# Performance work log

Hardware: AMD Instinct MI355X
Metric: run time of the kernel (lower is better)

The kernel has to match this reference:

```python
import jax, jax.numpy as jnp
import numpy as np
from jax.scipy.linalg import expm

HIDDEN = 1024
STATE = 64
INTER = 4096
EPS = 1e-06
DT_MIN, DT_MAX = 0.001, 0.1


def rmsnorm(x, w, eps=EPS):
    var = jnp.mean(x * x, axis=-1, keepdims=True)
    return x * jax.lax.rsqrt(var + eps) * w


def setup_inputs() -> dict:
    key = jax.random.key(0)
    ks = jax.random.split(key, 10)
    hidden_states = jax.random.normal(ks[0], (4, 2048, HIDDEN), dtype=jnp.float32)
    A = jax.random.normal(ks[1], (STATE, STATE), dtype=jnp.float32) * 0.01
    B = jax.random.normal(ks[2], (STATE, HIDDEN), dtype=jnp.float32) * 0.01
    C = jax.random.normal(ks[3], (HIDDEN, STATE), dtype=jnp.float32) * 0.01
    D = jnp.ones((HIDDEN,), dtype=jnp.float32)
    log_dt = jax.random.uniform(ks[4], (HIDDEN,), dtype=jnp.float32) * (np.log(DT_MAX) - np.log(DT_MIN)) + np.log(DT_MIN)
    s = 1.0 / np.sqrt(HIDDEN)
    w_gate = jax.random.uniform(ks[5], (INTER, HIDDEN), minval=-s, maxval=s, dtype=jnp.float32)
    w_up = jax.random.uniform(ks[6], (INTER, HIDDEN), minval=-s, maxval=s, dtype=jnp.float32)
    s2 = 1.0 / np.sqrt(INTER)
    w_down = jax.random.uniform(ks[7], (HIDDEN, INTER), minval=-s2, maxval=s2, dtype=jnp.float32)
    ln1_w = jnp.ones((HIDDEN,), dtype=jnp.float32)
    ln2_w = jnp.ones((HIDDEN,), dtype=jnp.float32)
    return {"hidden_states": hidden_states, "A": A, "B": B, "C": C, "D": D,
            "log_dt": log_dt, "w_gate": w_gate, "w_up": w_up, "w_down": w_down,
            "ln1_w": ln1_w, "ln2_w": ln2_w}


def ssm(x, A, B, C, D, log_dt):
    # x: (batch, seq, hidden)
    dt = jnp.exp(log_dt)                    # (hidden,)
    A_bar = expm(A * jnp.mean(dt))          # (state, state)
    B_bar = B * dt[None, :]                 # (state, hidden)

    def step(state, x_t):
        # state: (batch, state); x_t: (batch, hidden)
        state = state @ A_bar.T + x_t @ B_bar.T
        out = state @ C.T + D * x_t
        return state, out

    x_t = jnp.swapaxes(x, 0, 1)             # (seq, batch, hidden)
    init = jnp.zeros((x.shape[0], A.shape[0]), dtype=x.dtype)
    _, ys = jax.lax.scan(step, init, x_t)
    return jnp.swapaxes(ys, 0, 1)           # (batch, seq, hidden)


def reference(hidden_states, A, B, C, D, log_dt, w_gate, w_up, w_down, ln1_w, ln2_w):
    # pre-norm SSM mixer + residual
    residual = hidden_states
    h = rmsnorm(hidden_states, ln1_w)
    h = ssm(h, A, B, C, D, log_dt)
    h = residual + h
    # pre-norm SwiGLU FFN + residual
    residual = h
    hn = rmsnorm(h, ln2_w)
    gate = hn @ w_gate.T
    up = hn @ w_up.T
    ffn = (jax.nn.silu(gate) * up) @ w_down.T
    return residual + ffn
```

## Files before the change

kernel.cpp:

```cpp
#include <hip/hip_runtime.h>
#include <hip/hip_bf16.h>
#include <math.h>

typedef __attribute__((ext_vector_type(8))) short short8;
typedef __attribute__((ext_vector_type(4))) float f32x4;
typedef __attribute__((ext_vector_type(4))) int int4v;
typedef __attribute__((ext_vector_type(8))) int int8v;

__device__ __forceinline__ unsigned short f2b(float x) {
  union { float f; unsigned int u; } v; v.f = x;
  unsigned int r = v.u + 0x7fffu + ((v.u >> 16) & 1u);
  return (unsigned short)(r >> 16);
}
__device__ __forceinline__ float b2f(unsigned short u) {
  union { unsigned int u; float f; } v; v.u = ((unsigned int)u) << 16;
  return v.f;
}
__device__ __forceinline__ unsigned char f2f8_sw(float x) {
  float a = fabsf(x);
  unsigned char s = (x < 0.f) ? 0x80 : 0x00;
  if (a >= 464.f) return s | 0x7E;
  union { float f; unsigned u; } v; v.f = a;
  int e = (int)(v.u >> 23) - 127;
  if (e < -6) {
    int q = (int)rintf(a * 512.f);
    if (q >= 8) return s | 0x08;
    return s | (unsigned char)q;
  }
  unsigned mant = v.u & 0x7FFFFF;
  unsigned keep = mant >> 20;
  unsigned rest = mant & 0xFFFFF;
  if (rest > 0x80000u || (rest == 0x80000u && (keep & 1))) keep++;
  unsigned exp8 = (unsigned)(e + 7);
  if (keep == 8) { keep = 0; exp8++; }
  if (exp8 >= 15 && keep >= 7) return s | 0x7E;
  return s | (unsigned char)((exp8 << 3) | keep);
}
#if __has_builtin(__builtin_amdgcn_cvt_pk_fp8_f32)
__device__ __forceinline__ unsigned char f2f8(float x) {
  return (unsigned char)(__builtin_amdgcn_cvt_pk_fp8_f32(x, x, 0, false) & 0xFF);
}
__device__ __forceinline__ unsigned int f8pack4(float a, float b, float c, float d) {
  int w0 = __builtin_amdgcn_cvt_pk_fp8_f32(a, b, 0, false);
  return (unsigned int)__builtin_amdgcn_cvt_pk_fp8_f32(c, d, w0, true);
}
#else
__device__ __forceinline__ unsigned char f2f8(float x) { return f2f8_sw(x); }
__device__ __forceinline__ unsigned int f8pack4(float a, float b, float c, float d) {
  return (unsigned)f2f8_sw(a) | ((unsigned)f2f8_sw(b) << 8) |
         ((unsigned)f2f8_sw(c) << 16) | ((unsigned)f2f8_sw(d) << 24);
}
#endif
__device__ __forceinline__ void async_ld16(const void* g, void* l) {
  __builtin_amdgcn_global_load_lds(
      (const __attribute__((address_space(1))) void*)g,
      (__attribute__((address_space(3))) void*)l, 16, 0, 0);
}

__device__ __forceinline__ f32x4 mx8(int8v a, int8v b, f32x4 c) {
#if __has_builtin(__builtin_amdgcn_mfma_scale_f32_16x16x128_f8f6f4)
  return __builtin_amdgcn_mfma_scale_f32_16x16x128_f8f6f4(
      a, b, c, 0, 0, 0, 0x7F7F7F7F, 0, 0x7F7F7F7F);
#else
  union { int8v v; long l[4]; } av, bv; av.v = a; bv.v = b;
#pragma unroll
  for (int j = 0; j < 4; j++)
    c = __builtin_amdgcn_mfma_f32_16x16x32_fp8_fp8(av.l[j], bv.l[j], c, 0, 0, 0);
  return c;
#endif
}

__device__ __forceinline__ int8v rd8(const unsigned char* tb, int r, int q) {
  union { int8v v; int4v h[2]; } x;
  x.h[0] = *(const int4v*)(tb + (size_t)((r << 3) + ((2 * q)     ^ (r & 7))) * 16);
  x.h[1] = *(const int4v*)(tb + (size_t)((r << 3) + ((2 * q + 1) ^ (r & 7))) * 16);
  return x.v;
}

__global__ __launch_bounds__(1024) void prep_combo(
    const float* __restrict__ A, const float* __restrict__ logdt,
    float* __restrict__ Abar, float* __restrict__ A64,
    const float* __restrict__ B, const float* __restrict__ Cm,
    unsigned short* __restrict__ Bb, unsigned short* __restrict__ Cb) {
  __shared__ float red[16];
  __shared__ float Ms[4096], T[4096], P[4096];
  if (blockIdx.x != 0) {
    const size_t NB = 65536, NC = 65536;
    size_t base = (size_t)(blockIdx.x - 1) * 1024 + threadIdx.x;
    size_t stride = (size_t)(gridDim.x - 1) * 1024;
    for (size_t id = base; id < NB + NC; id += stride) {
      if (id < NB) { int k = (int)(id & 1023); Bb[id] = f2b(B[id] * expf(logdt[k])); }
      else Cb[id - NB] = f2b(Cm[id - NB]);
    }
    return;
  }
  const int tid = threadIdx.x;
  const int c = tid & 63;
  const int w = tid >> 6;
  float e = expf(logdt[tid]);
#pragma unroll
  for (int off = 32; off > 0; off >>= 1) e += __shfl_down(e, off);
  if (c == 0) red[w] = e;
  __syncthreads();
  if (tid == 0) {
    float s = 0.f;
    for (int i = 0; i < 16; i++) s += red[i];
    red[0] = s * (1.f / 1024.f);
  }
  __syncthreads();
  const float mdt = red[0];
  {
    float m0 = A[tid] * mdt, m1 = A[tid + 1024] * mdt,
          m2 = A[tid + 2048] * mdt, m3 = A[tid + 3072] * mdt;
    Ms[tid] = m0; Ms[tid + 1024] = m1; Ms[tid + 2048] = m2; Ms[tid + 3072] = m3;
    T[tid] = m0; T[tid + 1024] = m1; T[tid + 2048] = m2; T[tid + 3072] = m3;
    P[tid] = m0 + ((tid >> 6) == (tid & 63) ? 1.f : 0.f);
    P[tid + 1024] = m1 + (((tid + 1024) >> 6) == ((tid + 1024) & 63) ? 1.f : 0.f);
    P[tid + 2048] = m2 + (((tid + 2048) >> 6) == ((tid + 2048) & 63) ? 1.f : 0.f);
    P[tid + 3072] = m3 + (((tid + 3072) >> 6) == ((tid + 3072) & 63) ? 1.f : 0.f);
  }
  __syncthreads();
  float colM[64];
#pragma unroll
  for (int j = 0; j < 64; j++) colM[j] = Ms[j * 64 + c];
  for (int k = 2; k <= 6; k++) {
    const float inv = 1.f / (float)k;
    float accs[4];
#pragma unroll
    for (int i = 0; i < 4; i++) {
      const int r = w + 16 * i;
      const float4* Trow = (const float4*)(T + r * 64);
      float a0 = 0.f, a1 = 0.f, a2 = 0.f, a3 = 0.f;
#pragma unroll
      for (int j4 = 0; j4 < 16; j4++) {
        const float4 t = Trow[j4];
        a0 += t.x * colM[4 * j4 + 0]; a1 += t.y * colM[4 * j4 + 1];
        a2 += t.z * colM[4 * j4 + 2]; a3 += t.w * colM[4 * j4 + 3];
      }
      accs[i] = ((a0 + a1) + (a2 + a3)) * inv;
    }
    __syncthreads();
#pragma unroll
    for (int i = 0; i < 4; i++) {
      const int r = w + 16 * i;
      T[r * 64 + c] = accs[i];
      P[r * 64 + c] += accs[i];
    }
    __syncthreads();
  }
#pragma unroll
  for (int i = 0; i < 4; i++) {
    const int r = w + 16 * i;
    Abar[r * 64 + c] = P[r * 64 + c];
    T[r * 64 + c] = P[r * 64 + c];
  }
  __syncthreads();
  for (int sq = 0; sq < 6; sq++) {
    float colT[64];
#pragma unroll
    for (int j = 0; j < 64; j++) colT[j] = T[j * 64 + c];
    float accs[4];
#pragma unroll
    for (int i = 0; i < 4; i++) {
      const int r = w + 16 * i;
      const float4* Trow = (const float4*)(T + r * 64);
      float a0 = 0.f, a1 = 0.f, a2 = 0.f, a3 = 0.f;
#pragma unroll
      for (int j4 = 0; j4 < 16; j4++) {
        const float4 t = Trow[j4];
        a0 += t.x * colT[4 * j4 + 0]; a1 += t.y * colT[4 * j4 + 1];
        a2 += t.z * colT[4 * j4 + 2]; a3 += t.w * colT[4 * j4 + 3];
      }
      accs[i] = (a0 + a1) + (a2 + a3);
    }
    __syncthreads();
#pragma unroll
    for (int i = 0; i < 4; i++) T[(w + 16 * i) * 64 + c] = accs[i];
    __syncthreads();
  }
#pragma unroll
  for (int i = 0; i < 4; i++) {
    const int r = w + 16 * i;
    A64[r * 64 + c] = T[r * 64 + c];
  }
}

__global__ __launch_bounds__(256) void rmsnorm_bf16(
    const float* __restrict__ x, const float* __restrict__ w,
    unsigned short* __restrict__ out) {
  const size_t row = blockIdx.x;
  const int tid = threadIdx.x;
  const float4 v = ((const float4*)(x + row * 1024))[tid];
  float ss = v.x * v.x + v.y * v.y + v.z * v.z + v.w * v.w;
#pragma unroll
  for (int off = 32; off > 0; off >>= 1) ss += __shfl_down(ss, off);
  __shared__ float wsum[4];
  if ((tid & 63) == 0) wsum[tid >> 6] = ss;
  __syncthreads();
  const float tot = wsum[0] + wsum[1] + wsum[2] + wsum[3];
  const float rs = rsqrtf(tot * (1.f / 1024.f) + 1e-6f);
  const float4 wv = ((const float4*)w)[tid];
  ushort4 o;
  o.x = f2b(v.x * rs * wv.x); o.y = f2b(v.y * rs * wv.y);
  o.z = f2b(v.z * rs * wv.z); o.w = f2b(v.w * rs * wv.w);
  ((ushort4*)(out + row * 1024))[tid] = o;
}

__global__ __launch_bounds__(256) void rmsnorm_f8(
    const float* __restrict__ x, const float* __restrict__ w,
    unsigned int* __restrict__ out) {
  const size_t row = blockIdx.x;
  const int tid = threadIdx.x;
  const float4 v = ((const float4*)(x + row * 1024))[tid];
  float ss = v.x * v.x + v.y * v.y + v.z * v.z + v.w * v.w;
#pragma unroll
  for (int off = 32; off > 0; off >>= 1) ss += __shfl_down(ss, off);
  __shared__ float wsum[4];
  if ((tid & 63) == 0) wsum[tid >> 6] = ss;
  __syncthreads();
  const float tot = wsum[0] + wsum[1] + wsum[2] + wsum[3];
  const float rs = rsqrtf(tot * (1.f / 1024.f) + 1e-6f);
  const float4 wv = ((const float4*)w)[tid];
  out[row * 256 + tid] =
      f8pack4(v.x * rs * wv.x, v.y * rs * wv.y, v.z * rs * wv.z, v.w * rs * wv.w);
}

template <int STORE_S>
__global__ __launch_bounds__(256) void scan_combo(
    const float* __restrict__ U, const float* __restrict__ Abar,
    const float* __restrict__ carry, float* __restrict__ zend,
    unsigned short* __restrict__ S,
    const float* __restrict__ csrc, unsigned char* __restrict__ cdst, size_t ccount) {
  constexpr int SCAN_BLOCKS = 32;
  __shared__ float s[4][64];
  if (blockIdx.x >= SCAN_BLOCKS) {
    size_t base = (size_t)(blockIdx.x - SCAN_BLOCKS) * 256 + threadIdx.x;
    size_t stride = (size_t)(gridDim.x - SCAN_BLOCKS) * 256;
    for (size_t id = base; id < ccount; id += stride)
      cdst[id] = f2f8(csrc[id] * 64.f);
    return;
  }
  const int wave = threadIdx.x >> 6, i = threadIdx.x & 63;
  const int task = blockIdx.x * 4 + wave;
  const int b = task >> 5, c = task & 31;
  float a[64];
#pragma unroll
  for (int j = 0; j < 64; j++) a[j] = Abar[i * 64 + j];
  float cur = STORE_S ? carry[(b * 32 + c) * 64 + i] : 0.f;
  const float* Ub = U + ((size_t)(b * 2048 + c * 64)) * 64;
  for (int t = 0; t < 64; t++) {
    s[wave][i] = cur;
    __syncthreads();
    const float u = Ub[t * 64 + i];
    const float4* s4 = (const float4*)s[wave];
    float a0 = u, a1 = 0.f, a2 = 0.f, a3 = 0.f;
#pragma unroll
    for (int j = 0; j < 16; j++) {
      float4 v = s4[j];
      a0 += a[4 * j + 0] * v.x; a1 += a[4 * j + 1] * v.y;
      a2 += a[4 * j + 2] * v.z; a3 += a[4 * j + 3] * v.w;
    }
    cur = (a0 + a1) + (a2 + a3);
    __syncthreads();
    if (STORE_S) S[((size_t)(b * 2048 + c * 64 + t)) * 64 + i] = f2b(cur);
  }
  if (!STORE_S) zend[(b * 32 + c) * 64 + i] = cur;
}

__global__ __launch_bounds__(256) void carry_combo(
    const float* __restrict__ zend, const float* __restrict__ A64,
    float* __restrict__ carry,
    const float* __restrict__ csrc, unsigned char* __restrict__ cdst, size_t ccount) {
  __shared__ float s[4][64];
  if (blockIdx.x != 0) {
    size_t base = (size_t)(blockIdx.x - 1) * 256 + threadIdx.x;
    size_t stride = (size_t)(gridDim.x - 1) * 256;
    for (size_t id = base; id < ccount; id += stride)
      cdst[id] = f2f8(csrc[id] * 64.f);
    return;
  }
  const int b = threadIdx.x >> 6, i = threadIdx.x & 63;
  float a[64];
#pragma unroll
  for (int j = 0; j < 64; j++) a[j] = A64[i * 64 + j];
  float cur = 0.f;
  for (int c = 0; c < 32; c++) {
    carry[(b * 32 + c) * 64 + i] = cur;
    s[b][i] = cur;
    __syncthreads();
    const float z = zend[(b * 32 + c) * 64 + i];
    const float4* s4 = (const float4*)s[b];
    float a0 = z, a1 = 0.f, a2 = 0.f, a3 = 0.f;
#pragma unroll
    for (int j = 0; j < 16; j++) {
      float4 v = s4[j];
      a0 += a[4 * j + 0] * v.x; a1 += a[4 * j + 1] * v.y;
      a2 += a[4 * j + 2] * v.z; a3 += a[4 * j + 3] * v.w;
    }
    cur = (a0 + a1) + (a2 + a3);
    __syncthreads();
  }
}

template <int BM, int BN, int WAVES_M, int WAVES_N, int EPI>
__global__ void __launch_bounds__(256) gemm_bt(
    const unsigned short* __restrict__ X, const unsigned short* __restrict__ W,
    int M, int N, int K,
    float* __restrict__ outf, const unsigned short* __restrict__ e_b,
    const float* __restrict__ e_f, const float* __restrict__ e_d) {
  constexpr int BK = 64;
  constexpr int SM = BM / WAVES_M, SN = BN / WAVES_N;
  constexpr int TM = SM / 16, TN = SN / 16;
  __shared__ unsigned short aT[BM * BK];
  __shared__ unsigned short bT[BN * BK];
  const int tid = threadIdx.x;
  const int lane = tid & 63, wave = tid >> 6;
  const int wm = wave / WAVES_N, wn = wave % WAVES_N;
  const int lm = lane & 15, quad = lane >> 4;
  const long bm0 = (long)blockIdx.y * BM;
  const long bn0 = (long)blockIdx.x * BN;
  const int wb = tid & ~63;

  f32x4 acc[TM][TN];
#pragma unroll
  for (int i = 0; i < TM; i++)
#pragma unroll
    for (int j = 0; j < TN; j++) acc[i][j] = (f32x4){0.f, 0.f, 0.f, 0.f};

  for (int k0 = 0; k0 < K; k0 += BK) {
#pragma unroll
    for (int it = 0; it < (BM * 8) / 256; ++it) {
      int slot = it * 256 + tid;
      int r = slot >> 3, cp = slot & 7, c = cp ^ (r & 7);
      async_ld16(X + (bm0 + r) * (long)K + k0 + c * 8, aT + (it * 256 + wb) * 8);
    }
#pragma unroll
    for (int it = 0; it < (BN * 8) / 256; ++it) {
      int slot = it * 256 + tid;
      int r = slot >> 3, cp = slot & 7, c = cp ^ (r & 7);
      async_ld16(W + (bn0 + r) * (long)K + k0 + c * 8, bT + (it * 256 + wb) * 8);
    }
    __syncthreads();
#pragma unroll
    for (int kk = 0; kk < BK; kk += 32) {
      const int cch = (kk >> 3) + quad;
      short8 af[TM], bf[TN];
#pragma unroll
      for (int i = 0; i < TM; i++) {
        int r = wm * SM + i * 16 + lm;
        af[i] = *(const short8*)(aT + (r * 8 + (cch ^ (r & 7))) * 8);
      }
#pragma unroll
      for (int j = 0; j < TN; j++) {
        int r = wn * SN + j * 16 + lm;
        bf[j] = *(const short8*)(bT + (r * 8 + (cch ^ (r & 7))) * 8);
      }
#pragma unroll
      for (int i = 0; i < TM; i++)
#pragma unroll
        for (int j = 0; j < TN; j++)
          acc[i][j] = __builtin_amdgcn_mfma_f32_16x16x32_bf16(af[i], bf[j], acc[i][j], 0, 0, 0);
    }
    __syncthreads();
  }
#pragma unroll
  for (int i = 0; i < TM; i++) {
#pragma unroll
    for (int j = 0; j < TN; j++) {
#pragma unroll
      for (int r = 0; r < 4; r++) {
        const long m = bm0 + wm * SM + i * 16 + quad * 4 + r;
        const long n = bn0 + wn * SN + j * 16 + lm;
        const long idx = m * N + n;
        const float v = acc[i][j][r];
        if (EPI == 0) outf[idx] = v;
        else if (EPI == 4) outf[idx] = v + e_d[n] * b2f(e_b[idx]) + e_f[idx];
      }
    }
  }
}

__global__ void __launch_bounds__(256) gemm_gu(
    const unsigned char* __restrict__ X, const unsigned char* __restrict__ Wg,
    const unsigned char* __restrict__ Wu, int M, int N, int K,
    unsigned char* __restrict__ out8, float inv) {
  constexpr int BM = 128, BN = 64, BK = 128;
  constexpr int TM = 4, TN = 2;
  __shared__ __attribute__((aligned(16))) unsigned char aT[BM * BK];
  __shared__ __attribute__((aligned(16))) unsigned char gT[BN * BK];
  __shared__ __attribute__((aligned(16))) unsigned char uT[BN * BK];
  const int tid = threadIdx.x;
  const int lane = tid & 63, wave = tid >> 6;
  const int wm = wave >> 1, wn = wave & 1;
  const int lm = lane & 15, quad = lane >> 4;
  const long bm0 = (long)blockIdx.y * BM;
  const long bn0 = (long)blockIdx.x * BN;
  const int wb = tid & ~63;

  f32x4 accg[TM][TN], accu[TM][TN];
#pragma unroll
  for (int i = 0; i < TM; i++)
#pragma unroll
    for (int j = 0; j < TN; j++) {
      accg[i][j] = (f32x4){0.f, 0.f, 0.f, 0.f};
      accu[i][j] = (f32x4){0.f, 0.f, 0.f, 0.f};
    }

  for (int k0 = 0; k0 < K; k0 += BK) {
#pragma unroll
    for (int it = 0; it < 4; ++it) {
      int slot = it * 256 + tid;
      int r = slot >> 3, cp = slot & 7, c = cp ^ (r & 7);
      async_ld16(X + (bm0 + r) * (long)K + k0 + c * 16, aT + (it * 256 + wb) * 16);
    }
#pragma unroll
    for (int it = 0; it < 2; ++it) {
      int slot = it * 256 + tid;
      int r = slot >> 3, cp = slot & 7, c = cp ^ (r & 7);
      async_ld16(Wg + (bn0 + r) * (long)K + k0 + c * 16, gT + (it * 256 + wb) * 16);
    }
#pragma unroll
    for (int it = 0; it < 2; ++it) {
      int slot = it * 256 + tid;
      int r = slot >> 3, cp = slot & 7, c = cp ^ (r & 7);
      async_ld16(Wu + (bn0 + r) * (long)K + k0 + c * 16, uT + (it * 256 + wb) * 16);
    }
    __syncthreads();
    int8v a[TM], g[TN], u[TN];
#pragma unroll
    for (int i = 0; i < TM; i++) a[i] = rd8(aT, wm * 64 + i * 16 + lm, quad);
#pragma unroll
    for (int j = 0; j < TN; j++) {
      g[j] = rd8(gT, wn * 32 + j * 16 + lm, quad);
      u[j] = rd8(uT, wn * 32 + j * 16 + lm, quad);
    }
#pragma unroll
    for (int i = 0; i < TM; i++)
#pragma unroll
      for (int j = 0; j < TN; j++) {
        accg[i][j] = mx8(a[i], g[j], accg[i][j]);
        accu[i][j] = mx8(a[i], u[j], accu[i][j]);
      }
    __syncthreads();
  }
#pragma unroll
  for (int i = 0; i < TM; i++) {
#pragma unroll
    for (int j = 0; j < TN; j++) {
#pragma unroll
      for (int r = 0; r < 4; r++) {
        const long m = bm0 + wm * 64 + i * 16 + quad * 4 + r;
        const long n = bn0 + wn * 32 + j * 16 + lm;
        const float gg = accg[i][j][r] * inv;
        const float uu = accu[i][j][r] * inv;
        const float s = gg / (1.f + __expf(-gg));
        out8[m * N + n] = f2f8(s * uu);
      }
    }
  }
}

__global__ void __launch_bounds__(256) gemm_f8(
    const unsigned char* __restrict__ X, const unsigned char* __restrict__ W,
    int M, int N, int K,
    float* __restrict__ outf, const float* __restrict__ e_f, float inv) {
  constexpr int BM = 128, BN = 64, BK = 128;
  constexpr int TM = 4, TN = 2;
  __shared__ __attribute__((aligned(16))) unsigned char aT[BM * BK];
  __shared__ __attribute__((aligned(16))) unsigned char bT[BN * BK];
  const int tid = threadIdx.x;
  const int lane = tid & 63, wave = tid >> 6;
  const int wm = wave >> 1, wn = wave & 1;
  const int lm = lane & 15, quad = lane >> 4;
  const long bm0 = (long)blockIdx.y * BM;
  const long bn0 = (long)blockIdx.x * BN;
  const int wb = tid & ~63;

  f32x4 acc[TM][TN];
#pragma unroll
  for (int i = 0; i < TM; i++)
#pragma unroll
    for (int j = 0; j < TN; j++) acc[i][j] = (f32x4){0.f, 0.f, 0.f, 0.f};

  for (int k0 = 0; k0 < K; k0 += BK) {
#pragma unroll
    for (int it = 0; it < 4; ++it) {
      int slot = it * 256 + tid;
      int r = slot >> 3, cp = slot & 7, c = cp ^ (r & 7);
      async_ld16(X + (bm0 + r) * (long)K + k0 + c * 16, aT + (it * 256 + wb) * 16);
    }
#pragma unroll
    for (int it = 0; it < 2; ++it) {
      int slot = it * 256 + tid;
      int r = slot >> 3, cp = slot & 7, c = cp ^ (r & 7);
      async_ld16(W + (bn0 + r) * (long)K + k0 + c * 16, bT + (it * 256 + wb) * 16);
    }
    __syncthreads();
    int8v a[TM], b[TN];
#pragma unroll
    for (int i = 0; i < TM; i++) a[i] = rd8(aT, wm * 64 + i * 16 + lm, quad);
#pragma unroll
    for (int j = 0; j < TN; j++) b[j] = rd8(bT, wn * 32 + j * 16 + lm, quad);
#pragma unroll
    for (int i = 0; i < TM; i++)
#pragma unroll
      for (int j = 0; j < TN; j++)
        acc[i][j] = mx8(a[i], b[j], acc[i][j]);
    __syncthreads();
  }
#pragma unroll
  for (int i = 0; i < TM; i++) {
#pragma unroll
    for (int j = 0; j < TN; j++) {
#pragma unroll
      for (int r = 0; r < 4; r++) {
        const long m = bm0 + wm * 64 + i * 16 + quad * 4 + r;
        const long n = bn0 + wn * 32 + j * 16 + lm;
        const long idx = m * N + n;
        outf[idx] = acc[i][j][r] * inv + e_f[idx];
      }
    }
  }
}

extern "C" void kernel_launch(void* const* d_in, const int* in_sizes, int n_in,
                              void* d_out, int out_size, void* d_ws, size_t ws_size,
                              hipStream_t stream) {
  const float* x     = (const float*)d_in[0];
  const float* A     = (const float*)d_in[1];
  const float* B     = (const float*)d_in[2];
  const float* C     = (const float*)d_in[3];
  const float* D     = (const float*)d_in[4];
  const float* logdt = (const float*)d_in[5];
  const float* wg    = (const float*)d_in[6];
  const float* wu    = (const float*)d_in[7];
  const float* wd    = (const float*)d_in[8];
  const float* ln1   = (const float*)d_in[9];
  const float* ln2   = (const float*)d_in[10];
  float* out = (float*)d_out;

  char* p = (char*)d_ws;
  auto alloc = [&](size_t bytes) { char* q = p; p += (bytes + 255) & ~(size_t)255; return q; };
  float* Abar  = (float*)alloc(64 * 64 * 4);
  float* A64   = (float*)alloc(64 * 64 * 4);
  float* zend  = (float*)alloc(4 * 32 * 64 * 4);
  float* carry = (float*)alloc(4 * 32 * 64 * 4);
  float* U     = (float*)alloc((size_t)8192 * 64 * 4);
  unsigned short* S    = (unsigned short*)alloc((size_t)8192 * 64 * 2);
  unsigned short* Bb   = (unsigned short*)alloc((size_t)64 * 1024 * 2);
  unsigned short* Cb   = (unsigned short*)alloc((size_t)1024 * 64 * 2);
  unsigned char*  wg8  = (unsigned char*)alloc((size_t)4096 * 1024);
  unsigned char*  wu8  = (unsigned char*)alloc((size_t)4096 * 1024);
  unsigned char*  wd8  = (unsigned char*)alloc((size_t)1024 * 4096);
  unsigned short* xnb  = (unsigned short*)alloc((size_t)8192 * 1024 * 2);
  unsigned char*  hn8  = (unsigned char*)alloc((size_t)8192 * 1024);
  float* h             = (float*)alloc((size_t)8192 * 1024 * 4);
  unsigned char*  act8 = (unsigned char*)alloc((size_t)8192 * 4096);

  const size_t NWG = (size_t)4096 * 1024;

  prep_combo<<<33, 1024, 0, stream>>>(A, logdt, Abar, A64, B, C, Bb, Cb);
  rmsnorm_bf16<<<8192, 256, 0, stream>>>(x, ln1, xnb);
  gemm_bt<32, 64, 2, 2, 0><<<dim3(1, 256), 256, 0, stream>>>(
      xnb, Bb, 8192, 64, 1024, U, nullptr, nullptr, nullptr);
  scan_combo<0><<<32 + 1024, 256, 0, stream>>>(
      U, Abar, nullptr, zend, S, wg, wg8, NWG);
  carry_combo<<<1 + 1024, 256, 0, stream>>>(zend, A64, carry, wu, wu8, NWG);
  scan_combo<1><<<32 + 1024, 256, 0, stream>>>(
      U, Abar, carry, zend, S, wd, wd8, NWG);
  gemm_bt<128, 128, 2, 2, 4><<<dim3(8, 64), 256, 0, stream>>>(
      S, Cb, 8192, 1024, 64, h, xnb, x, D);
  rmsnorm_f8<<<8192, 256, 0, stream>>>(h, ln2, (unsigned int*)hn8);
  gemm_gu<<<dim3(64, 64), 256, 0, stream>>>(
      hn8, wg8, wu8, 8192, 4096, 1024, act8, 1.f / 64.f);
  gemm_f8<<<dim3(16, 64), 256, 0, stream>>>(
      act8, wd8, 8192, 1024, 4096, out, h, 1.f / 64.f);
}
```

Measured before the change: 430.7 us.

## Load two K-slices per barrier in gate/up GEMM and remap blocks for XCD locality

```diff
diff --git a/kernel.cpp b/kernel.cpp
--- a/kernel.cpp
+++ b/kernel.cpp
@@ -386,15 +386,17 @@
     unsigned char* __restrict__ out8, float inv) {
   constexpr int BM = 128, BN = 64, BK = 128;
   constexpr int TM = 4, TN = 2;
-  __shared__ __attribute__((aligned(16))) unsigned char aT[BM * BK];
-  __shared__ __attribute__((aligned(16))) unsigned char gT[BN * BK];
-  __shared__ __attribute__((aligned(16))) unsigned char uT[BN * BK];
+  __shared__ __attribute__((aligned(16))) unsigned char aT[2][BM * BK];
+  __shared__ __attribute__((aligned(16))) unsigned char gT[2][BN * BK];
+  __shared__ __attribute__((aligned(16))) unsigned char uT[2][BN * BK];
   const int tid = threadIdx.x;
   const int lane = tid & 63, wave = tid >> 6;
   const int wm = wave >> 1, wn = wave & 1;
   const int lm = lane & 15, quad = lane >> 4;
-  const long bm0 = (long)blockIdx.y * BM;
-  const long bn0 = (long)blockIdx.x * BN;
+  const int lid = blockIdx.y * 64 + blockIdx.x;
+  const int sw = (lid & 7) * 512 + (lid >> 3);
+  const long bm0 = (long)(sw >> 6) * BM;
+  const long bn0 = (long)(sw & 63) * BN;
   const int wb = tid & ~63;
 
   f32x4 accg[TM][TN], accu[TM][TN];
@@ -406,41 +408,43 @@
       accu[i][j] = (f32x4){0.f, 0.f, 0.f, 0.f};
     }
 
-  for (int k0 = 0; k0 < K; k0 += BK) {
-#pragma unroll
-    for (int it = 0; it < 4; ++it) {
-      int slot = it * 256 + tid;
-      int r = slot >> 3, cp = slot & 7, c = cp ^ (r & 7);
-      async_ld16(X + (bm0 + r) * (long)K + k0 + c * 16, aT + (it * 256 + wb) * 16);
-    }
-#pragma unroll
-    for (int it = 0; it < 2; ++it) {
-      int slot = it * 256 + tid;
-      int r = slot >> 3, cp = slot & 7, c = cp ^ (r & 7);
-      async_ld16(Wg + (bn0 + r) * (long)K + k0 + c * 16, gT + (it * 256 + wb) * 16);
-    }
-#pragma unroll
-    for (int it = 0; it < 2; ++it) {
-      int slot = it * 256 + tid;
-      int r = slot >> 3, cp = slot & 7, c = cp ^ (r & 7);
-      async_ld16(Wu + (bn0 + r) * (long)K + k0 + c * 16, uT + (it * 256 + wb) * 16);
-    }
-    __syncthreads();
-    int8v a[TM], g[TN], u[TN];
-#pragma unroll
-    for (int i = 0; i < TM; i++) a[i] = rd8(aT, wm * 64 + i * 16 + lm, quad);
-#pragma unroll
-    for (int j = 0; j < TN; j++) {
-      g[j] = rd8(gT, wn * 32 + j * 16 + lm, quad);
-      u[j] = rd8(uT, wn * 32 + j * 16 + lm, quad);
-    }
-#pragma unroll
-    for (int i = 0; i < TM; i++)
+  for (int k0 = 0; k0 < K; k0 += 2 * BK) {
+#pragma unroll
+    for (int h = 0; h < 2; ++h) {
+      const long kh = k0 + h * BK;
+#pragma unroll
+      for (int it = 0; it < 4; ++it) {
+        int slot = it * 256 + tid;
+        int r = slot >> 3, cp = slot & 7, c = cp ^ (r & 7);
+        async_ld16(X + (bm0 + r) * (long)K + kh + c * 16, &aT[h][(it * 256 + wb) * 16]);
+      }
+#pragma unroll
+      for (int it = 0; it < 2; ++it) {
+        int slot = it * 256 + tid;
+        int r = slot >> 3, cp = slot & 7, c = cp ^ (r & 7);
+        async_ld16(Wg + (bn0 + r) * (long)K + kh + c * 16, &gT[h][(it * 256 + wb) * 16]);
+        async_ld16(Wu + (bn0 + r) * (long)K + kh + c * 16, &uT[h][(it * 256 + wb) * 16]);
+      }
+    }
+    __syncthreads();
+#pragma unroll
+    for (int h = 0; h < 2; ++h) {
+      int8v a[TM], g[TN], u[TN];
+#pragma unroll
+      for (int i = 0; i < TM; i++) a[i] = rd8(aT[h], wm * 64 + i * 16 + lm, quad);
 #pragma unroll
       for (int j = 0; j < TN; j++) {
-        accg[i][j] = mx8(a[i], g[j], accg[i][j]);
-        accu[i][j] = mx8(a[i], u[j], accu[i][j]);
-      }
+        g[j] = rd8(gT[h], wn * 32 + j * 16 + lm, quad);
+        u[j] = rd8(uT[h], wn * 32 + j * 16 + lm, quad);
+      }
+#pragma unroll
+      for (int i = 0; i < TM; i++)
+#pragma unroll
+        for (int j = 0; j < TN; j++) {
+          accg[i][j] = mx8(a[i], g[j], accg[i][j]);
+          accu[i][j] = mx8(a[i], u[j], accu[i][j]);
+        }
+    }
     __syncthreads();
   }
 #pragma unroll
@@ -472,8 +476,10 @@
   const int lane = tid & 63, wave = tid >> 6;
   const int wm = wave >> 1, wn = wave & 1;
   const int lm = lane & 15, quad = lane >> 4;
-  const long bm0 = (long)blockIdx.y * BM;
-  const long bn0 = (long)blockIdx.x * BN;
+  const int lid = blockIdx.y * 16 + blockIdx.x;
+  const int sw = (lid & 7) * 128 + (lid >> 3);
+  const long bm0 = (long)(sw >> 4) * BM;
+  const long bn0 = (long)(sw & 15) * BN;
   const int wb = tid & ~63;
 
   f32x4 acc[TM][TN];
```

Result: no change. 433.5 us (+0.7%).

## Fuse first RMSNorm into prep kernel, drop scan barriers, recompute residual epilogue

Applied to the files above, without the earlier changes.

```diff
diff --git a/kernel.cpp b/kernel.cpp
--- a/kernel.cpp
+++ b/kernel.cpp
@@ -81,20 +81,43 @@
     const float* __restrict__ A, const float* __restrict__ logdt,
     float* __restrict__ Abar, float* __restrict__ A64,
     const float* __restrict__ B, const float* __restrict__ Cm,
-    unsigned short* __restrict__ Bb, unsigned short* __restrict__ Cb) {
+    unsigned short* __restrict__ Bb, unsigned short* __restrict__ Cb,
+    const float* __restrict__ x, const float* __restrict__ w1,
+    unsigned short* __restrict__ xnb, float* __restrict__ rs_out) {
   __shared__ float red[16];
   __shared__ float Ms[4096], T[4096], P[4096];
+  __shared__ float wsum2[16];
+  const int tid = threadIdx.x;
+  if (blockIdx.x >= 33) {
+    const int sub = tid >> 8, t = tid & 255;
+    const size_t row = (size_t)(blockIdx.x - 33) * 4 + sub;
+    const float4 v = ((const float4*)(x + row * 1024))[t];
+    float ss = v.x * v.x + v.y * v.y + v.z * v.z + v.w * v.w;
+#pragma unroll
+    for (int off = 32; off > 0; off >>= 1) ss += __shfl_down(ss, off);
+    if ((t & 63) == 0) wsum2[(sub << 2) | (t >> 6)] = ss;
+    __syncthreads();
+    const float tot = wsum2[sub << 2] + wsum2[(sub << 2) | 1] +
+                      wsum2[(sub << 2) | 2] + wsum2[(sub << 2) | 3];
+    const float rs = rsqrtf(tot * (1.f / 1024.f) + 1e-6f);
+    if (t == 0) rs_out[row] = rs;
+    const float4 wv = ((const float4*)w1)[t];
+    ushort4 o;
+    o.x = f2b(v.x * rs * wv.x); o.y = f2b(v.y * rs * wv.y);
+    o.z = f2b(v.z * rs * wv.z); o.w = f2b(v.w * rs * wv.w);
+    ((ushort4*)(xnb + row * 1024))[t] = o;
+    return;
+  }
   if (blockIdx.x != 0) {
     const size_t NB = 65536, NC = 65536;
-    size_t base = (size_t)(blockIdx.x - 1) * 1024 + threadIdx.x;
-    size_t stride = (size_t)(gridDim.x - 1) * 1024;
+    size_t base = (size_t)(blockIdx.x - 1) * 1024 + tid;
+    const size_t stride = 32 * 1024;
     for (size_t id = base; id < NB + NC; id += stride) {
       if (id < NB) { int k = (int)(id & 1023); Bb[id] = f2b(B[id] * expf(logdt[k])); }
       else Cb[id - NB] = f2b(Cm[id - NB]);
     }
     return;
   }
-  const int tid = threadIdx.x;
   const int c = tid & 63;
   const int w = tid >> 6;
   float e = expf(logdt[tid]);
@@ -183,27 +206,6 @@
     const int r = w + 16 * i;
     A64[r * 64 + c] = T[r * 64 + c];
   }
-}
-
-__global__ __launch_bounds__(256) void rmsnorm_bf16(
-    const float* __restrict__ x, const float* __restrict__ w,
-    unsigned short* __restrict__ out) {
-  const size_t row = blockIdx.x;
-  const int tid = threadIdx.x;
-  const float4 v = ((const float4*)(x + row * 1024))[tid];
-  float ss = v.x * v.x + v.y * v.y + v.z * v.z + v.w * v.w;
-#pragma unroll
-  for (int off = 32; off > 0; off >>= 1) ss += __shfl_down(ss, off);
-  __shared__ float wsum[4];
-  if ((tid & 63) == 0) wsum[tid >> 6] = ss;
-  __syncthreads();
-  const float tot = wsum[0] + wsum[1] + wsum[2] + wsum[3];
-  const float rs = rsqrtf(tot * (1.f / 1024.f) + 1e-6f);
-  const float4 wv = ((const float4*)w)[tid];
-  ushort4 o;
-  o.x = f2b(v.x * rs * wv.x); o.y = f2b(v.y * rs * wv.y);
-  o.z = f2b(v.z * rs * wv.z); o.w = f2b(v.w * rs * wv.w);
-  ((ushort4*)(out + row * 1024))[tid] = o;
 }
 
 __global__ __launch_bounds__(256) void rmsnorm_f8(
@@ -248,10 +250,11 @@
   for (int j = 0; j < 64; j++) a[j] = Abar[i * 64 + j];
   float cur = STORE_S ? carry[(b * 32 + c) * 64 + i] : 0.f;
   const float* Ub = U + ((size_t)(b * 2048 + c * 64)) * 64;
+  float u = Ub[i];
   for (int t = 0; t < 64; t++) {
     s[wave][i] = cur;
-    __syncthreads();
-    const float u = Ub[t * 64 + i];
+    float u_next = 0.f;
+    if (t + 1 < 64) u_next = Ub[(t + 1) * 64 + i];
     const float4* s4 = (const float4*)s[wave];
     float a0 = u, a1 = 0.f, a2 = 0.f, a3 = 0.f;
 #pragma unroll
@@ -261,8 +264,8 @@
       a2 += a[4 * j + 2] * v.z; a3 += a[4 * j + 3] * v.w;
     }
     cur = (a0 + a1) + (a2 + a3);
-    __syncthreads();
     if (STORE_S) S[((size_t)(b * 2048 + c * 64 + t)) * 64 + i] = f2b(cur);
+    u = u_next;
   }
   if (!STORE_S) zend[(b * 32 + c) * 64 + i] = cur;
 }
@@ -284,11 +287,12 @@
 #pragma unroll
   for (int j = 0; j < 64; j++) a[j] = A64[i * 64 + j];
   float cur = 0.f;
+  float z = zend[(b * 32 + 0) * 64 + i];
   for (int c = 0; c < 32; c++) {
     carry[(b * 32 + c) * 64 + i] = cur;
     s[b][i] = cur;
-    __syncthreads();
-    const float z = zend[(b * 32 + c) * 64 + i];
+    float z_next = 0.f;
+    if (c + 1 < 32) z_next = zend[(b * 32 + c + 1) * 64 + i];
     const float4* s4 = (const float4*)s[b];
     float a0 = z, a1 = 0.f, a2 = 0.f, a3 = 0.f;
 #pragma unroll
@@ -298,7 +302,7 @@
       a2 += a[4 * j + 2] * v.z; a3 += a[4 * j + 3] * v.w;
     }
     cur = (a0 + a1) + (a2 + a3);
-    __syncthreads();
+    z = z_next;
   }
 }
 
@@ -306,8 +310,9 @@
 __global__ void __launch_bounds__(256) gemm_bt(
     const unsigned short* __restrict__ X, const unsigned short* __restrict__ W,
     int M, int N, int K,
-    float* __restrict__ outf, const unsigned short* __restrict__ e_b,
-    const float* __restrict__ e_f, const float* __restrict__ e_d) {
+    float* __restrict__ outf, const float* __restrict__ e_f,
+    const float* __restrict__ e_d, const float* __restrict__ e_w,
+    const float* __restrict__ e_r) {
   constexpr int BK = 64;
   constexpr int SM = BM / WAVES_M, SN = BN / WAVES_N;
   constexpr int TM = SM / 16, TN = SN / 16;
@@ -374,7 +379,8 @@
         const long idx = m * N + n;
         const float v = acc[i][j][r];
         if (EPI == 0) outf[idx] = v;
-        else if (EPI == 4) outf[idx] = v + e_d[n] * b2f(e_b[idx]) + e_f[idx];
+        else if (EPI == 5)
+          outf[idx] = v + e_f[idx] * (1.f + e_d[n] * e_w[n] * e_r[m]);
       }
     }
   }
@@ -545,6 +551,7 @@
   float* A64   = (float*)alloc(64 * 64 * 4);
   float* zend  = (float*)alloc(4 * 32 * 64 * 4);
   float* carry = (float*)alloc(4 * 32 * 64 * 4);
+  float* rs    = (float*)alloc((size_t)8192 * 4);
   float* U     = (float*)alloc((size_t)8192 * 64 * 4);
   unsigned short* S    = (unsigned short*)alloc((size_t)8192 * 64 * 2);
   unsigned short* Bb   = (unsigned short*)alloc((size_t)64 * 1024 * 2);
@@ -559,17 +566,17 @@
 
   const size_t NWG = (size_t)4096 * 1024;
 
-  prep_combo<<<33, 1024, 0, stream>>>(A, logdt, Abar, A64, B, C, Bb, Cb);
-  rmsnorm_bf16<<<8192, 256, 0, stream>>>(x, ln1, xnb);
+  prep_combo<<<33 + 2048, 1024, 0, stream>>>(
+      A, logdt, Abar, A64, B, C, Bb, Cb, x, ln1, xnb, rs);
   gemm_bt<32, 64, 2, 2, 0><<<dim3(1, 256), 256, 0, stream>>>(
-      xnb, Bb, 8192, 64, 1024, U, nullptr, nullptr, nullptr);
+      xnb, Bb, 8192, 64, 1024, U, nullptr, nullptr, nullptr, nullptr);
   scan_combo<0><<<32 + 1024, 256, 0, stream>>>(
       U, Abar, nullptr, zend, S, wg, wg8, NWG);
   carry_combo<<<1 + 1024, 256, 0, stream>>>(zend, A64, carry, wu, wu8, NWG);
   scan_combo<1><<<32 + 1024, 256, 0, stream>>>(
       U, Abar, carry, zend, S, wd, wd8, NWG);
-  gemm_bt<128, 128, 2, 2, 4><<<dim3(8, 64), 256, 0, stream>>>(
-      S, Cb, 8192, 1024, 64, h, xnb, x, D);
+  gemm_bt<128, 128, 2, 2, 5><<<dim3(8, 64), 256, 0, stream>>>(
+      S, Cb, 8192, 1024, 64, h, x, D, ln1, rs);
   rmsnorm_f8<<<8192, 256, 0, stream>>>(h, ln2, (unsigned int*)hn8);
   gemm_gu<<<dim3(64, 64), 256, 0, stream>>>(
       hn8, wg8, wu8, 8192, 4096, 1024, act8, 1.f / 64.f);
```

Result: faster. 397.5 us (-7.7%).
